# Kernel tuning notes

Measured on AMD Instinct MI355X. Metric: run time of the kernel, lower is better.

The kernel has to match this reference:

```python
import jax, jax.numpy as jnp
import numpy as np

B, T, D = 4, 2048, 1024
C_BIAS = 0.0  # init kwarg c
LN_EPS = 1e-5


def setup_inputs() -> dict:
    key = jax.random.key(0)
    ks = jax.random.split(key, 8)
    s = 1.0 / np.sqrt(D)
    return {
        "x": jax.random.normal(ks[0], (B, T, D), dtype=jnp.float32),
        "l": jax.random.randint(ks[1], (B,), 1, T + 1),  # lengths in [1, T]
        "Wq": jax.random.normal(ks[2], (D, D), dtype=jnp.float32) * s,
        "Wk": jax.random.normal(ks[3], (D, D), dtype=jnp.float32) * s,
        "Wv": jax.random.normal(ks[4], (D, D), dtype=jnp.float32) * s,
        "Wo": jax.random.normal(ks[5], (D, D), dtype=jnp.float32) * s,
        "bo": jnp.zeros((D,), dtype=jnp.float32),
        "gamma": jnp.ones((D,), dtype=jnp.float32),
        "beta": jnp.zeros((D,), dtype=jnp.float32),
    }


def reference(x, l, Wq, Wk, Wv, Wo, bo, gamma, beta):
    # LayerNorm over last dim
    mu = jnp.mean(x, axis=-1, keepdims=True)
    var = jnp.mean(jnp.square(x - mu), axis=-1, keepdims=True)
    x_norm = (x - mu) * jax.lax.rsqrt(var + LN_EPS) * gamma + beta

    # QKV projections (torch Linear: y = x @ W.T, no bias)
    q = jnp.einsum("btd,ed->bte", x_norm, Wq)
    k = jnp.einsum("btd,ed->bte", x_norm, Wk)
    v = jnp.einsum("btd,ed->bte", x_norm, Wv)

    scale = 1.0 / jnp.sqrt(jnp.float32(D))
    scores = C_BIAS + jnp.einsum("bid,bjd->bij", q, k) * scale  # [B,T,T]

    # Mask is applied along the ROW (dim 1) axis, and softmax is over dim 1
    # (faithful to the original: mask.unsqueeze(2) + Softmax(dim=1)).
    valid_rows = jnp.arange(T)[None, :] < l[:, None]  # [B,T]
    scores = jnp.where(valid_rows[:, :, None], scores, -jnp.inf)
    attn = jax.nn.softmax(scores, axis=1)  # normalize over rows

    y = x + jnp.einsum("bij,bjd->bid", attn, v)
    out = jax.nn.relu(jnp.einsum("btd,ed->bte", y, Wo) + bo)
    return out
```

## Files before the change

kernel.cpp:

```cpp
#include <hip/hip_runtime.h>
#include <hip/hip_fp16.h>

typedef unsigned short u16;
typedef __attribute__((ext_vector_type(8))) short bf16x8;
typedef __attribute__((ext_vector_type(4))) float f32x4;

#define T_SEQ 2048
#define DIM 1024
#define NB 4
#define NCH 16

__device__ __forceinline__ u16 f2bf(float f) {
  union { float f; unsigned u; } c; c.f = f;
  unsigned r = c.u + 0x7fffu + ((c.u >> 16) & 1u);
  return (u16)(r >> 16);
}

__device__ __forceinline__ void gload_lds16(const void* g, void* l) {
  __builtin_amdgcn_global_load_lds((const __attribute__((address_space(1))) void*)g,
                                   (__attribute__((address_space(3))) void*)l, 16, 0, 0);
}

__global__ __launch_bounds__(256) void ln_kernel(const float* __restrict__ x,
                                                 const float* __restrict__ gamma,
                                                 const float* __restrict__ beta,
                                                 u16* __restrict__ xn) {
  const int row = blockIdx.x;
  const int tid = threadIdx.x;
  const float4 v = *(const float4*)(x + (size_t)row * DIM + tid * 4);
  float s  = v.x + v.y + v.z + v.w;
  float ss = v.x * v.x + v.y * v.y + v.z * v.z + v.w * v.w;
#pragma unroll
  for (int o = 32; o > 0; o >>= 1) { s += __shfl_down(s, o); ss += __shfl_down(ss, o); }
  __shared__ float rs[4], rss[4];
  const int wid = tid >> 6, lane = tid & 63;
  if (lane == 0) { rs[wid] = s; rss[wid] = ss; }
  __syncthreads();
  s  = rs[0] + rs[1] + rs[2] + rs[3];
  ss = rss[0] + rss[1] + rss[2] + rss[3];
  const float mu = s * (1.f / DIM);
  const float var = ss * (1.f / DIM) - mu * mu;
  const float rstd = rsqrtf(var + 1e-5f);
  const float4 g  = *(const float4*)(gamma + tid * 4);
  const float4 be = *(const float4*)(beta + tid * 4);
  ushort4 o;
  o.x = f2bf((v.x - mu) * rstd * g.x + be.x);
  o.y = f2bf((v.y - mu) * rstd * g.y + be.y);
  o.z = f2bf((v.z - mu) * rstd * g.z + be.z);
  o.w = f2bf((v.w - mu) * rstd * g.w + be.w);
  *(ushort4*)(xn + (size_t)row * DIM + tid * 4) = o;
}

__global__ __launch_bounds__(256) void wcvt4(const float* __restrict__ wq,
                                             const float* __restrict__ wk,
                                             const float* __restrict__ wv,
                                             const float* __restrict__ wo,
                                             u16* __restrict__ dqk,
                                             u16* __restrict__ dv,
                                             u16* __restrict__ dw) {
  const int sel = blockIdx.x >> 10;
  const size_t t = (size_t)(blockIdx.x & 1023) * 256 + threadIdx.x;
  const float* w = (sel == 0) ? wq : (sel == 1) ? wk : (sel == 2) ? wv : wo;
  u16* d = (sel == 0) ? dqk : (sel == 1) ? (dqk + 1048576) : (sel == 2) ? dv : dw;
  const float4 v = *(const float4*)(w + t * 4);
  ushort4 u; u.x = f2bf(v.x); u.y = f2bf(v.y); u.z = f2bf(v.z); u.w = f2bf(v.w);
  *(ushort4*)(d + t * 4) = u;
}

template <int EPI, int MSK>
__global__ __launch_bounds__(256, 4) void gemm97(
    const u16* __restrict__ A, const u16* __restrict__ B, void* __restrict__ Cv,
    int K, int lda, int ldb, int ldc,
    long sA, long sB, long sC, float scale,
    const float* __restrict__ aux, long sAux,
    const int* __restrict__ lptr, float* __restrict__ mpQ, float* __restrict__ zpQ) {
  __shared__ __align__(16) u16 As[128 * 64];
  __shared__ __align__(16) u16 Bs[128 * 64];
  const int bz = blockIdx.z;
  const u16* Ab = A + (size_t)bz * sA;
  const u16* Bb = B + (size_t)bz * sB;

  const int nb = gridDim.x * gridDim.y;
  int bid = blockIdx.y * gridDim.x + blockIdx.x;
  bid = (bid & 7) * (nb >> 3) + (bid >> 3);
  const int gx = gridDim.x;
  const int tileN = (bid % gx) * 128;
  const int tileM = (bid / gx) * 128;

  const int t = threadIdx.x;

  if constexpr (MSK == 1) {
    if (tileM >= lptr[bz]) return;
  }
  if constexpr (MSK == 3) {
    if (((tileM & (T_SEQ - 1)) >= lptr[tileM >> 11]) && tileN < DIM) return;
  }
  if constexpr (MSK == 2) {
    if (tileM >= lptr[bz]) {
      const float* xb = aux + (size_t)bz * sAux;
      u16* yo = (u16*)Cv + (size_t)bz * sC;
      for (int e = t; e < (128 * 128) / 8; e += 256) {
        const int row = tileM + (e >> 4);
        const int col = tileN + ((e & 15) << 3);
        const float4 v0 = *(const float4*)(xb + (size_t)row * ldc + col);
        const float4 v1 = *(const float4*)(xb + (size_t)row * ldc + col + 4);
        ushort4 o0; o0.x = f2bf(v0.x); o0.y = f2bf(v0.y); o0.z = f2bf(v0.z); o0.w = f2bf(v0.w);
        ushort4 o1; o1.x = f2bf(v1.x); o1.y = f2bf(v1.y); o1.z = f2bf(v1.z); o1.w = f2bf(v1.w);
        *(ushort4*)(yo + (size_t)row * ldc + col) = o0;
        *(ushort4*)(yo + (size_t)row * ldc + col + 4) = o1;
      }
      return;
    }
  }

  const int lane = t & 63;
  const int wid = t >> 6;
  const int wm = wid >> 1, wn = wid & 1;

  const int r0s = t >> 3;
  const int sch = ((t & 7) ^ (r0s & 7)) * 8;

  const int frow = lane & 15, kg = lane >> 4, f7 = lane & 7;

  f32x4 acc[4][4] = {};

  for (int k0 = 0; k0 < K; k0 += 64) {
    if (k0) __syncthreads();
#pragma unroll
    for (int i = 0; i < 4; ++i) {
      const int e = i * 256 + t;
      const int row = i * 32 + r0s;
      gload_lds16(Ab + (size_t)(tileM + row) * lda + k0 + sch, &As[e * 8]);
      gload_lds16(Bb + (size_t)(tileN + row) * ldb + k0 + sch, &Bs[e * 8]);
    }
    __syncthreads();
#pragma unroll
    for (int h = 0; h < 2; ++h) {
      const int cs = (((h * 4 + kg) ^ f7)) * 8;
      bf16x8 af[4], bf[4];
#pragma unroll
      for (int i = 0; i < 4; ++i)
        af[i] = *(const bf16x8*)&As[(wm * 64 + i * 16 + frow) * 64 + cs];
#pragma unroll
      for (int j = 0; j < 4; ++j)
        bf[j] = *(const bf16x8*)&Bs[(wn * 64 + j * 16 + frow) * 64 + cs];
#pragma unroll
      for (int i = 0; i < 4; ++i)
#pragma unroll
        for (int j = 0; j < 4; ++j)
          acc[i][j] = __builtin_amdgcn_mfma_f32_16x16x32_bf16(af[i], bf[j], acc[i][j], 0, 0, 0);
    }
  }

  const int r0 = tileM + wm * 64 + (kg << 2);
  const int c0 = tileN + wn * 64 + frow;
#pragma unroll
  for (int i = 0; i < 4; ++i)
#pragma unroll
    for (int j = 0; j < 4; ++j)
#pragma unroll
      for (int r = 0; r < 4; ++r) {
        const int row = r0 + i * 16 + r, col = c0 + j * 16;
        const size_t idx = (size_t)row * ldc + col;
        float v = acc[i][j][r];
        if constexpr (EPI == 0) {
          ((u16*)Cv + (size_t)bz * sC)[idx] = f2bf(v);
        } else if constexpr (EPI == 1) {
          ((__half*)Cv + (size_t)bz * sC)[idx] = __float2half(v * scale);
        } else if constexpr (EPI == 2) {
          v += (aux + (size_t)bz * sAux)[idx];
          ((u16*)Cv + (size_t)bz * sC)[idx] = f2bf(v);
        } else {
          v += aux[col];
          ((float*)Cv + (size_t)bz * sC)[idx] = fmaxf(v, 0.f);
        }
      }

  if constexpr (EPI == 1) {
    const int L = lptr[bz];
    __shared__ float2 red[2][2][4][16];
    float Ms[4], Zs[4];
#pragma unroll
    for (int j = 0; j < 4; ++j) {
      float mj = -3e38f;
#pragma unroll
      for (int i = 0; i < 4; ++i)
#pragma unroll
        for (int r = 0; r < 4; ++r) {
          const int row = r0 + i * 16 + r;
          if (row < L) mj = fmaxf(mj, acc[i][j][r] * scale);
        }
      mj = fmaxf(mj, __shfl_xor(mj, 16, 64));
      mj = fmaxf(mj, __shfl_xor(mj, 32, 64));
      float zj = 0.f;
#pragma unroll
      for (int i = 0; i < 4; ++i)
#pragma unroll
        for (int r = 0; r < 4; ++r) {
          const int row = r0 + i * 16 + r;
          if (row < L) zj += __expf(acc[i][j][r] * scale - mj);
        }
      zj += __shfl_xor(zj, 16, 64);
      zj += __shfl_xor(zj, 32, 64);
      Ms[j] = mj; Zs[j] = zj;
    }
    if (lane < 16) {
#pragma unroll
      for (int j = 0; j < 4; ++j) red[wm][wn][j][frow] = make_float2(Ms[j], Zs[j]);
    }
    __syncthreads();
    if (wm == 0 && lane < 16) {
#pragma unroll
      for (int j = 0; j < 4; ++j) {
        const float2 a = red[0][wn][j][frow];
        const float2 b = red[1][wn][j][frow];
        const float M = fmaxf(a.x, b.x);
        const float Z = a.y * __expf(a.x - M) + b.y * __expf(b.x - M);
        const int col = tileN + wn * 64 + j * 16 + frow;
        const size_t o = ((size_t)(tileM >> 7) * NB + bz) * T_SEQ + col;
        mpQ[o] = M; zpQ[o] = Z;
      }
    }
  }
}

__global__ __launch_bounds__(256) void colreduce_comb(const float* __restrict__ mp,
                                                      const float* __restrict__ zp,
                                                      const int* __restrict__ l,
                                                      float* __restrict__ m,
                                                      float* __restrict__ rz) {
  const int b = blockIdx.y;
  const int j = blockIdx.x * 256 + threadIdx.x;
  const int L = l[b];
  float M = -3e38f, Z = 0.f;
  for (int c = 0; c < NCH && (c << 7) < L; ++c) {
    const size_t o = ((size_t)c * NB + b) * T_SEQ + j;
    const float mc = mp[o], zc = zp[o];
    const float nm = fmaxf(M, mc);
    Z = Z * __expf(M - nm) + zc * __expf(mc - nm);
    M = nm;
  }
  m[b * T_SEQ + j] = M;
  rz[b * T_SEQ + j] = 1.f / Z;
}

__global__ __launch_bounds__(256) void pbuild(const __half* __restrict__ S,
                                              const int* __restrict__ l,
                                              const float* __restrict__ m,
                                              const float* __restrict__ rz,
                                              u16* __restrict__ P) {
  const int b = blockIdx.x >> 11;
  const int i = blockIdx.x & (T_SEQ - 1);
  const int L = l[b];
  if (i >= ((L + 127) & ~127)) return;
  const int j0 = threadIdx.x * 8;
  const size_t off = ((size_t)blockIdx.x << 11) + j0;
  ushort4 o0, o1;
  if (i < L) {
    const __half* sp = S + off;
    const float* mp = m + b * T_SEQ + j0;
    const float* zp = rz + b * T_SEQ + j0;
    u16 tmp[8];
#pragma unroll
    for (int tt = 0; tt < 8; ++tt)
      tmp[tt] = f2bf(__expf(__half2float(sp[tt]) - mp[tt]) * zp[tt]);
    o0 = make_ushort4(tmp[0], tmp[1], tmp[2], tmp[3]);
    o1 = make_ushort4(tmp[4], tmp[5], tmp[6], tmp[7]);
  } else {
    o0 = make_ushort4(0, 0, 0, 0);
    o1 = make_ushort4(0, 0, 0, 0);
  }
  *(ushort4*)(P + off) = o0;
  *(ushort4*)(P + off + 4) = o1;
}

extern "C" void kernel_launch(void* const* d_in, const int* in_sizes, int n_in,
                              void* d_out, int out_size, void* d_ws, size_t ws_size,
                              hipStream_t stream) {
  (void)in_sizes; (void)n_in; (void)out_size; (void)ws_size;
  const float* x     = (const float*)d_in[0];
  const int*   l     = (const int*)d_in[1];
  const float* Wq    = (const float*)d_in[2];
  const float* Wk    = (const float*)d_in[3];
  const float* Wv    = (const float*)d_in[4];
  const float* Wo    = (const float*)d_in[5];
  const float* bo    = (const float*)d_in[6];
  const float* gamma = (const float*)d_in[7];
  const float* beta  = (const float*)d_in[8];

  char* ws = (char*)d_ws;
  const size_t MiB = 1024 * 1024;
  u16* xn   = (u16*)(ws);
  u16* wqkb = (u16*)(ws + 16 * MiB);
  u16* wvb  = (u16*)(ws + 20 * MiB);
  u16* wob  = (u16*)(ws + 22 * MiB);
  u16* QKb  = (u16*)(ws + 24 * MiB);
  u16* Vt   = (u16*)(ws + 56 * MiB);
  float* mpart = (float*)(ws + 20 * MiB);
  float* zpart = (float*)(ws + 20 * MiB + 512 * 1024);
  float* mb  = (float*)(ws + 72 * MiB);
  float* rzb = (float*)(ws + 72 * MiB + 32 * 1024);
  u16* Pb = QKb;
  u16* yb = xn;
  __half* S = (__half*)d_out;
  float* outp = (float*)d_out;

  const long TD = (long)T_SEQ * DIM, TT = (long)T_SEQ * T_SEQ;
  const long TQK = (long)T_SEQ * 2048;

  ln_kernel<<<NB * T_SEQ, 256, 0, stream>>>(x, gamma, beta, xn);
  wcvt4<<<4096, 256, 0, stream>>>(Wq, Wk, Wv, Wo, wqkb, wvb, wob);

  gemm97<0, 3><<<dim3(16, 64, 1), 256, 0, stream>>>(
      xn, wqkb, QKb, DIM, DIM, DIM, 2048, 0, 0, 0, 0.f, nullptr, 0,
      l, nullptr, nullptr);
  gemm97<0, 0><<<dim3(64, 8, 1), 256, 0, stream>>>(
      wvb, xn, Vt, DIM, DIM, DIM, 8192, 0, 0, 0, 0.f, nullptr, 0,
      nullptr, nullptr, nullptr);
  gemm97<1, 1><<<dim3(16, 16, NB), 256, 0, stream>>>(
      QKb, QKb + 1024, S, DIM, 2048, 2048, T_SEQ, TQK, TQK, TT, 0.03125f,
      nullptr, 0, l, mpart, zpart);
  colreduce_comb<<<dim3(T_SEQ / 256, NB), 256, 0, stream>>>(mpart, zpart, l, mb, rzb);
  pbuild<<<NB * T_SEQ, 256, 0, stream>>>(S, l, mb, rzb, Pb);
  gemm97<2, 2><<<dim3(8, 16, NB), 256, 0, stream>>>(
      Pb, Vt, yb, T_SEQ, T_SEQ, 8192, DIM, TT, 2048, TD, 0.f, x, TD,
      l, nullptr, nullptr);
  gemm97<3, 0><<<dim3(8, 64, 1), 256, 0, stream>>>(
      yb, wob, outp, DIM, DIM, DIM, DIM, 0, 0, 0, 0.f, bo, 0,
      nullptr, nullptr, nullptr);
}
```

Before: 206.8 us.

## Fold Wq·Wk into one matrix and fuse softmax-prob build into PV GEMM

```diff
diff --git a/kernel.cpp b/kernel.cpp
--- a/kernel.cpp
+++ b/kernel.cpp
@@ -51,20 +51,46 @@
   *(ushort4*)(xn + (size_t)row * DIM + tid * 4) = o;
 }
 
-__global__ __launch_bounds__(256) void wcvt4(const float* __restrict__ wq,
-                                             const float* __restrict__ wk,
-                                             const float* __restrict__ wv,
+__global__ __launch_bounds__(256) void wcvt2(const float* __restrict__ wv,
                                              const float* __restrict__ wo,
-                                             u16* __restrict__ dqk,
                                              u16* __restrict__ dv,
                                              u16* __restrict__ dw) {
   const int sel = blockIdx.x >> 10;
   const size_t t = (size_t)(blockIdx.x & 1023) * 256 + threadIdx.x;
-  const float* w = (sel == 0) ? wq : (sel == 1) ? wk : (sel == 2) ? wv : wo;
-  u16* d = (sel == 0) ? dqk : (sel == 1) ? (dqk + 1048576) : (sel == 2) ? dv : dw;
+  const float* w = sel ? wo : wv;
+  u16* d = sel ? dw : dv;
   const float4 v = *(const float4*)(w + t * 4);
   ushort4 u; u.x = f2bf(v.x); u.y = f2bf(v.y); u.z = f2bf(v.z); u.w = f2bf(v.w);
   *(ushort4*)(d + t * 4) = u;
+}
+
+__global__ __launch_bounds__(256) void wtrT(const float* __restrict__ wq,
+                                            const float* __restrict__ wk,
+                                            u16* __restrict__ dqT,
+                                            u16* __restrict__ dkT) {
+  __shared__ u16 tile[64][72];
+  const float* w = blockIdx.z ? wk : wq;
+  u16* d = blockIdx.z ? dkT : dqT;
+  const int f0 = blockIdx.y * 64, d0 = blockIdx.x * 64;
+  const int t = threadIdx.x;
+  const int tr = t >> 4, tc = (t & 15) * 4;
+#pragma unroll
+  for (int p = 0; p < 4; ++p) {
+    const float4 v = *(const float4*)(w + (size_t)(f0 + tr + 16 * p) * DIM + d0 + tc);
+    tile[tr + 16 * p][tc]     = f2bf(v.x);
+    tile[tr + 16 * p][tc + 1] = f2bf(v.y);
+    tile[tr + 16 * p][tc + 2] = f2bf(v.z);
+    tile[tr + 16 * p][tc + 3] = f2bf(v.w);
+  }
+  __syncthreads();
+#pragma unroll
+  for (int p = 0; p < 4; ++p) {
+    const int dr = tr + 16 * p;
+    ushort4 u;
+    u.x = tile[tc][dr]; u.y = tile[tc + 1][dr];
+    u.z = tile[tc + 2][dr]; u.w = tile[tc + 3][dr];
+    *(ushort4*)(d + (size_t)(d0 + dr) * DIM + f0 + tc) = u;
+  }
 }
 
 template <int EPI, int MSK>
@@ -72,7 +98,7 @@
     const u16* __restrict__ A, const u16* __restrict__ B, void* __restrict__ Cv,
     int K, int lda, int ldb, int ldc,
     long sA, long sB, long sC, float scale,
-    const float* __restrict__ aux, long sAux,
+    const float* __restrict__ bias,
     const int* __restrict__ lptr, float* __restrict__ mpQ, float* __restrict__ zpQ) {
   __shared__ __align__(16) u16 As[128 * 64];
   __shared__ __align__(16) u16 Bs[128 * 64];
@@ -92,25 +118,8 @@
   if constexpr (MSK == 1) {
     if (tileM >= lptr[bz]) return;
   }
-  if constexpr (MSK == 3) {
-    if (((tileM & (T_SEQ - 1)) >= lptr[tileM >> 11]) && tileN < DIM) return;
-  }
-  if constexpr (MSK == 2) {
-    if (tileM >= lptr[bz]) {
-      const float* xb = aux + (size_t)bz * sAux;
-      u16* yo = (u16*)Cv + (size_t)bz * sC;
-      for (int e = t; e < (128 * 128) / 8; e += 256) {
-        const int row = tileM + (e >> 4);
-        const int col = tileN + ((e & 15) << 3);
-        const float4 v0 = *(const float4*)(xb + (size_t)row * ldc + col);
-        const float4 v1 = *(const float4*)(xb + (size_t)row * ldc + col + 4);
-        ushort4 o0; o0.x = f2bf(v0.x); o0.y = f2bf(v0.y); o0.z = f2bf(v0.z); o0.w = f2bf(v0.w);
-        ushort4 o1; o1.x = f2bf(v1.x); o1.y = f2bf(v1.y); o1.z = f2bf(v1.z); o1.w = f2bf(v1.w);
-        *(ushort4*)(yo + (size_t)row * ldc + col) = o0;
-        *(ushort4*)(yo + (size_t)row * ldc + col + 4) = o1;
-      }
-      return;
-    }
+  if constexpr (MSK == 4) {
+    if ((tileM & (T_SEQ - 1)) >= lptr[tileM >> 11]) return;
   }
 
   const int lane = t & 63;
@@ -167,11 +176,8 @@
           ((u16*)Cv + (size_t)bz * sC)[idx] = f2bf(v);
         } else if constexpr (EPI == 1) {
           ((__half*)Cv + (size_t)bz * sC)[idx] = __float2half(v * scale);
-        } else if constexpr (EPI == 2) {
-          v += (aux + (size_t)bz * sAux)[idx];
-          ((u16*)Cv + (size_t)bz * sC)[idx] = f2bf(v);
         } else {
-          v += aux[col];
+          v += bias[col];
           ((float*)Cv + (size_t)bz * sC)[idx] = fmaxf(v, 0.f);
         }
       }
@@ -222,6 +228,117 @@
       }
     }
   }
+}
+
+__global__ __launch_bounds__(256, 4) void gemm_pv(
+    const __half* __restrict__ Sg, const u16* __restrict__ Vt,
+    u16* __restrict__ C, const float* __restrict__ x,
+    const int* __restrict__ lptr,
+    const float* __restrict__ mb, const float* __restrict__ rzb) {
+  __shared__ __align__(16) u16 As[128 * 64];
+  __shared__ __align__(16) u16 Bs[128 * 64];
+  const int bz = blockIdx.z;
+  const __half* Ab = Sg + (size_t)bz * T_SEQ * T_SEQ;
+  const u16* Bb = Vt + (size_t)bz * T_SEQ;
+  const float* mp = mb + bz * T_SEQ;
+  const float* rp = rzb + bz * T_SEQ;
+
+  const int nb = gridDim.x * gridDim.y;
+  int bid = blockIdx.y * gridDim.x + blockIdx.x;
+  bid = (bid & 7) * (nb >> 3) + (bid >> 3);
+  const int gx = gridDim.x;
+  const int tileN = (bid % gx) * 128;
+  const int tileM = (bid / gx) * 128;
+  const int t = threadIdx.x;
+  const int L = lptr[bz];
+
+  if (tileM >= L) {
+    const float* xb = x + (size_t)bz * T_SEQ * DIM;
+    u16* yo = C + (size_t)bz * T_SEQ * DIM;
+    for (int e = t; e < (128 * 128) / 8; e += 256) {
+      const int row = tileM + (e >> 4);
+      const int col = tileN + ((e & 15) << 3);
+      const float4 v0 = *(const float4*)(xb + (size_t)row * DIM + col);
+      const float4 v1 = *(const float4*)(xb + (size_t)row * DIM + col + 4);
+      ushort4 o0; o0.x = f2bf(v0.x); o0.y = f2bf(v0.y); o0.z = f2bf(v0.z); o0.w = f2bf(v0.w);
+      ushort4 o1; o1.x = f2bf(v1.x); o1.y = f2bf(v1.y); o1.z = f2bf(v1.z); o1.w = f2bf(v1.w);
+      *(ushort4*)(yo + (size_t)row * DIM + col) = o0;
+      *(ushort4*)(yo + (size_t)row * DIM + col + 4) = o1;
+    }
+    return;
+  }
+
+  const int lane = t & 63;
+  const int wid = t >> 6;
+  const int wm = wid >> 1, wn = wid & 1;
+
+  const int r0s = t >> 3;
+  const int sch = ((t & 7) ^ (r0s & 7)) * 8;
+  const int asrc = (t & 7) * 8;
+  const int frow = lane & 15, kg = lane >> 4, f7 = lane & 7;
+
+  f32x4 acc[4][4] = {};
+
+  for (int k0 = 0; k0 < T_SEQ; k0 += 64) {
+    if (k0) __syncthreads();
+#pragma unroll
+    for (int i = 0; i < 4; ++i) {
+      const int row = i * 32 + r0s;
+      gload_lds16(Bb + (size_t)(tileN + row) * 8192 + k0 + sch, &Bs[(i * 256 + t) * 8]);
+    }
+    const int j0 = k0 + asrc;
+    float mv[8], zv[8];
+    *(float4*)&mv[0] = *(const float4*)(mp + j0);
+    *(float4*)&mv[4] = *(const float4*)(mp + j0 + 4);
+    *(float4*)&zv[0] = *(const float4*)(rp + j0);
+    *(float4*)&zv[4] = *(const float4*)(rp + j0 + 4);
+#pragma unroll
+    for (int i = 0; i < 4; ++i) {
+      const int row = i * 32 + r0s;
+      const int grow = tileM + row;
+      const float4 sv = *(const float4*)(Ab + (size_t)grow * T_SEQ + j0);
+      const __half* hp = (const __half*)&sv;
+      bf16x8 pv = {0, 0, 0, 0, 0, 0, 0, 0};
+      if (grow < L) {
+#pragma unroll
+        for (int q = 0; q < 8; ++q)
+          pv[q] = (short)f2bf(__expf(__half2float(hp[q]) - mv[q]) * zv[q]);
+      }
+      *(bf16x8*)&As[row * 64 + ((t & 7) ^ (row & 7)) * 8] = pv;
+    }
+    __syncthreads();
+#pragma unroll
+    for (int h = 0; h < 2; ++h) {
+      const int cs = (((h * 4 + kg) ^ f7)) * 8;
+      bf16x8 af[4], bf[4];
+#pragma unroll
+      for (int i = 0; i < 4; ++i)
+        af[i] = *(const bf16x8*)&As[(wm * 64 + i * 16 + frow) * 64 + cs];
+#pragma unroll
+      for (int j = 0; j < 4; ++j)
+        bf[j] = *(const bf16x8*)&Bs[(wn * 64 + j * 16 + frow) * 64 + cs];
+#pragma unroll
+      for (int i = 0; i < 4; ++i)
+#pragma unroll
+        for (int j = 0; j < 4; ++j)
+          acc[i][j] = __builtin_amdgcn_mfma_f32_16x16x32_bf16(af[i], bf[j], acc[i][j], 0, 0, 0);
+    }
+  }
+
+  const float* xb = x + (size_t)bz * T_SEQ * DIM;
+  u16* yo = C + (size_t)bz * T_SEQ * DIM;
+  const int r0 = tileM + wm * 64 + (kg << 2);
+  const int c0 = tileN + wn * 64 + frow;
+#pragma unroll
+  for (int i = 0; i < 4; ++i)
+#pragma unroll
+    for (int j = 0; j < 4; ++j)
+#pragma unroll
+      for (int r = 0; r < 4; ++r) {
+        const int row = r0 + i * 16 + r, col = c0 + j * 16;
+        const size_t idx = (size_t)row * DIM + col;
+        yo[idx] = f2bf(acc[i][j][r] + xb[idx]);
+      }
 }
 
 __global__ __launch_bounds__(256) void colreduce_comb(const float* __restrict__ mp,
@@ -244,36 +361,6 @@
   rz[b * T_SEQ + j] = 1.f / Z;
 }
 
-__global__ __launch_bounds__(256) void pbuild(const __half* __restrict__ S,
-                                              const int* __restrict__ l,
-                                              const float* __restrict__ m,
-                                              const float* __restrict__ rz,
-                                              u16* __restrict__ P) {
-  const int b = blockIdx.x >> 11;
-  const int i = blockIdx.x & (T_SEQ - 1);
-  const int L = l[b];
-  if (i >= ((L + 127) & ~127)) return;
-  const int j0 = threadIdx.x * 8;
-  const size_t off = ((size_t)blockIdx.x << 11) + j0;
-  ushort4 o0, o1;
-  if (i < L) {
-    const __half* sp = S + off;
-    const float* mp = m + b * T_SEQ + j0;
-    const float* zp = rz + b * T_SEQ + j0;
-    u16 tmp[8];
-#pragma unroll
-    for (int tt = 0; tt < 8; ++tt)
-      tmp[tt] = f2bf(__expf(__half2float(sp[tt]) - mp[tt]) * zp[tt]);
-    o0 = make_ushort4(tmp[0], tmp[1], tmp[2], tmp[3]);
-    o1 = make_ushort4(tmp[4], tmp[5], tmp[6], tmp[7]);
-  } else {
-    o0 = make_ushort4(0, 0, 0, 0);
-    o1 = make_ushort4(0, 0, 0, 0);
-  }
-  *(ushort4*)(P + off) = o0;
-  *(ushort4*)(P + off + 4) = o1;
-}
-
 extern "C" void kernel_launch(void* const* d_in, const int* in_sizes, int n_in,
                               void* d_out, int out_size, void* d_ws, size_t ws_size,
                               hipStream_t stream) {
@@ -290,42 +377,43 @@
 
   char* ws = (char*)d_ws;
   const size_t MiB = 1024 * 1024;
-  u16* xn   = (u16*)(ws);
-  u16* wqkb = (u16*)(ws + 16 * MiB);
-  u16* wvb  = (u16*)(ws + 20 * MiB);
-  u16* wob  = (u16*)(ws + 22 * MiB);
-  u16* QKb  = (u16*)(ws + 24 * MiB);
-  u16* Vt   = (u16*)(ws + 56 * MiB);
-  float* mpart = (float*)(ws + 20 * MiB);
-  float* zpart = (float*)(ws + 20 * MiB + 512 * 1024);
-  float* mb  = (float*)(ws + 72 * MiB);
-  float* rzb = (float*)(ws + 72 * MiB + 32 * 1024);
-  u16* Pb = QKb;
+  u16* xn  = (u16*)(ws);
+  u16* wvb = (u16*)(ws + 16 * MiB);
+  u16* wob = (u16*)(ws + 18 * MiB);
+  u16* wqT = (u16*)(ws + 20 * MiB);
+  u16* wkT = (u16*)(ws + 22 * MiB);
+  u16* MpT = (u16*)(ws + 24 * MiB);
+  u16* Qp  = (u16*)(ws + 26 * MiB);
+  u16* Vt  = (u16*)(ws + 42 * MiB);
+  float* mpart = (float*)(ws + 58 * MiB);
+  float* zpart = (float*)(ws + 58 * MiB + 512 * 1024);
+  float* mb  = (float*)(ws + 59 * MiB);
+  float* rzb = (float*)(ws + 59 * MiB + 32 * 1024);
   u16* yb = xn;
   __half* S = (__half*)d_out;
   float* outp = (float*)d_out;
 
   const long TD = (long)T_SEQ * DIM, TT = (long)T_SEQ * T_SEQ;
-  const long TQK = (long)T_SEQ * 2048;
 
   ln_kernel<<<NB * T_SEQ, 256, 0, stream>>>(x, gamma, beta, xn);
-  wcvt4<<<4096, 256, 0, stream>>>(Wq, Wk, Wv, Wo, wqkb, wvb, wob);
-
-  gemm97<0, 3><<<dim3(16, 64, 1), 256, 0, stream>>>(
-      xn, wqkb, QKb, DIM, DIM, DIM, 2048, 0, 0, 0, 0.f, nullptr, 0,
+  wcvt2<<<2048, 256, 0, stream>>>(Wv, Wo, wvb, wob);
+  wtrT<<<dim3(16, 16, 2), 256, 0, stream>>>(Wq, Wk, wqT, wkT);
+
+  gemm97<0, 0><<<dim3(8, 8, 1), 256, 0, stream>>>(
+      wkT, wqT, MpT, DIM, DIM, DIM, DIM, 0, 0, 0, 0.f, nullptr,
+      nullptr, nullptr, nullptr);
+  gemm97<0, 4><<<dim3(8, 64, 1), 256, 0, stream>>>(
+      xn, MpT, Qp, DIM, DIM, DIM, DIM, 0, 0, 0, 0.f, nullptr,
       l, nullptr, nullptr);
   gemm97<0, 0><<<dim3(64, 8, 1), 256, 0, stream>>>(
-      wvb, xn, Vt, DIM, DIM, DIM, 8192, 0, 0, 0, 0.f, nullptr, 0,
+      wvb, xn, Vt, DIM, DIM, DIM, 8192, 0, 0, 0, 0.f, nullptr,
       nullptr, nullptr, nullptr);
   gemm97<1, 1><<<dim3(16, 16, NB), 256, 0, stream>>>(
-      QKb, QKb + 1024, S, DIM, 2048, 2048, T_SEQ, TQK, TQK, TT, 0.03125f,
-      nullptr, 0, l, mpart, zpart);
+      Qp, xn, S, DIM, DIM, DIM, T_SEQ, TD, TD, TT, 0.03125f, nullptr,
+      l, mpart, zpart);
   colreduce_comb<<<dim3(T_SEQ / 256, NB), 256, 0, stream>>>(mpart, zpart, l, mb, rzb);
-  pbuild<<<NB * T_SEQ, 256, 0, stream>>>(S, l, mb, rzb, Pb);
-  gemm97<2, 2><<<dim3(8, 16, NB), 256, 0, stream>>>(
-      Pb, Vt, yb, T_SEQ, T_SEQ, 8192, DIM, TT, 2048, TD, 0.f, x, TD,
-      l, nullptr, nullptr);
+  gemm_pv<<<dim3(8, 16, NB), 256, 0, stream>>>(S, Vt, yb, x, l, mb, rzb);
   gemm97<3, 0><<<dim3(8, 64, 1), 256, 0, stream>>>(
-      yb, wob, outp, DIM, DIM, DIM, DIM, 0, 0, 0, 0.f, bo, 0,
+      yb, wob, outp, DIM, DIM, DIM, DIM, 0, 0, 0, 0.f, bo,
       nullptr, nullptr, nullptr);
 }
```

Result: slower. 249.1 us (+20.4%).
